# Kernel tuning notes

Hardware: AMD Instinct MI355X
Metric: run time of the kernel (lower is better)

The kernel has to match this reference:

```python
import jax, jax.numpy as jnp
import numpy as np
from jax import lax

B, LE, LD = 16, 512, 256
D, H, DFF = 512, 8, 2048
ENC_IN, DEC_IN, MARK, CO = 7, 7, 4, 7
NE, ND = 3, 2
TOPK = int((D // H) * 0.25)  # 16, from ProbSparseMultiheadAttention


def layer_norm(x, p):
    m = jnp.mean(x, -1, keepdims=True)
    v = jnp.mean((x - m) ** 2, -1, keepdims=True)
    return (x - m) / jnp.sqrt(v + 1e-5) * p[0] + p[1]


def attn(q, k, v, W, b, mask=None, topk=None):
    # W: [4, D, D] (q,k,v,o), b: [4, D]
    Bq, Lq, _ = q.shape
    dk = D // H
    Q = (q @ W[0] + b[0]).reshape(Bq, Lq, H, dk)
    K = (k @ W[1] + b[1]).reshape(Bq, -1, H, dk)
    V = (v @ W[2] + b[2]).reshape(Bq, -1, H, dk)
    s = jnp.einsum('bqhd,bkhd->bhqk', Q, K) / jnp.sqrt(jnp.float32(dk))
    if mask is not None:
        s = s + mask * (-1e9)
    if topk is not None:
        # ProbSparse: keep only top-k key scores per query before softmax
        kth = lax.top_k(s, topk)[0][..., -1:]
        s = jnp.where(s >= kth, s, -1e9)
    w = jax.nn.softmax(s, axis=-1)
    o = jnp.einsum('bhqk,bkhd->bqhd', w, V).reshape(Bq, Lq, D)
    return o @ W[3] + b[3]


def conv_distill(x, w, cb, g, bb):
    # x: [B, L, D]; circular-pad conv1d(k=3, pad=2) + BN(batch stats) + ELU + maxpool(k3,s2,p1)
    xc = jnp.transpose(x, (0, 2, 1))
    xp = jnp.pad(xc, ((0, 0), (0, 0), (2, 2)), mode='wrap')
    y = lax.conv_general_dilated(xp, w, (1,), 'VALID', dimension_numbers=('NCH', 'OIH', 'NCH')) + cb[None, :, None]
    m = jnp.mean(y, (0, 2), keepdims=True)
    v = jnp.var(y, (0, 2), keepdims=True)
    y = (y - m) / jnp.sqrt(v + 1e-5) * g[None, :, None] + bb[None, :, None]
    y = jax.nn.elu(y)
    y = lax.reduce_window(y, -jnp.inf, lax.max, (1, 1, 3), (1, 1, 2), ((0, 0), (0, 0), (1, 1)))
    return jnp.transpose(y, (0, 2, 1))


def setup_inputs() -> dict:
    key = jax.random.key(0)
    ks = iter(jax.random.split(key, 64))
    def nrm(shape, s=0.02):
        return jax.random.normal(next(ks), shape, dtype=jnp.float32) * s
    def ln_p(*lead):
        return jnp.stack([jnp.ones(lead + (D,), jnp.float32), jnp.zeros(lead + (D,), jnp.float32)], axis=len(lead))
    return {
        'x_enc': nrm((B, LE, ENC_IN), 1.0),
        'x_mark_enc': nrm((B, LE, MARK), 1.0),
        'x_dec': nrm((B, LD, DEC_IN), 1.0),
        'x_mark_dec': nrm((B, LD, MARK), 1.0),
        'enc_vw': nrm((ENC_IN, D)), 'enc_vb': jnp.zeros((D,)),
        'enc_mw': nrm((MARK, D)), 'enc_mb': jnp.zeros((D,)),
        'dec_vw': nrm((DEC_IN, D)), 'dec_vb': jnp.zeros((D,)),
        'dec_mw': nrm((MARK, D)), 'dec_mb': jnp.zeros((D,)),
        'eW': nrm((NE, 4, D, D)), 'eb': jnp.zeros((NE, 4, D)),
        'effw1': nrm((NE, D, DFF)), 'effb1': jnp.zeros((NE, DFF)),
        'effw2': nrm((NE, DFF, D)), 'effb2': jnp.zeros((NE, D)),
        'eln1': ln_p(NE), 'eln2': ln_p(NE),
        'cw': nrm((NE - 1, D, D, 3)), 'cb': jnp.zeros((NE - 1, D)),
        'cbn_g': jnp.ones((NE - 1, D)), 'cbn_b': jnp.zeros((NE - 1, D)),
        'enc_norm': ln_p(),
        'dsW': nrm((ND, 4, D, D)), 'dsb': jnp.zeros((ND, 4, D)),
        'dcW': nrm((ND, 4, D, D)), 'dcb': jnp.zeros((ND, 4, D)),
        'dffw1': nrm((ND, D, DFF)), 'dffb1': jnp.zeros((ND, DFF)),
        'dffw2': nrm((ND, DFF, D)), 'dffb2': jnp.zeros((ND, D)),
        'dln': ln_p(ND, 3),
        'dec_norm': ln_p(),
        'fcw': nrm((D, CO)), 'fcb': jnp.zeros((CO,)),
    }


def reference(x_enc, x_mark_enc, x_dec, x_mark_dec, enc_vw, enc_vb, enc_mw, enc_mb,
              dec_vw, dec_vb, dec_mw, dec_mb, eW, eb, effw1, effb1, effw2, effb2,
              eln1, eln2, cw, cb, cbn_g, cbn_b, enc_norm, dsW, dsb, dcW, dcb,
              dffw1, dffb1, dffw2, dffb2, dln, dec_norm, fcw, fcb):
    # embedding: value projection + temporal-mark projection
    x = x_enc @ enc_vw + enc_vb + x_mark_enc @ enc_mw + enc_mb
    # encoder: ProbSparse attn layers with conv distillation after the first NE-1
    for i in range(NE):
        a = attn(x, x, x, eW[i], eb[i], topk=TOPK)
        x = layer_norm(x + a, eln1[i])
        f = jax.nn.relu(x @ effw1[i] + effb1[i]) @ effw2[i] + effb2[i]
        x = layer_norm(x + f, eln2[i])
        if i < NE - 1:
            x = conv_distill(x, cw[i], cb[i], cbn_g[i], cbn_b[i])
    mem = layer_norm(x, enc_norm)
    # decoder
    y = x_dec @ dec_vw + dec_vb + x_mark_dec @ dec_mw + dec_mb
    cmask = jnp.triu(jnp.ones((LD, LD), jnp.float32), 1)[None, None]
    for i in range(ND):
        a = attn(y, y, y, dsW[i], dsb[i], mask=cmask)
        y = layer_norm(y + a, dln[i, 0])
        a = attn(y, mem, mem, dcW[i], dcb[i])
        y = layer_norm(y + a, dln[i, 1])
        f = jax.nn.relu(y @ dffw1[i] + dffb1[i]) @ dffw2[i] + dffb2[i]
        y = layer_norm(y + f, dln[i, 2])
    y = layer_norm(y, dec_norm)
    return y @ fcw + fcb
```

## Files before the change

### kernel.cpp

```cpp
#include <hip/hip_runtime.h>
#include <hip/hip_bf16.h>


#define DM 512
#define DK 64

using bf16 = __hip_bfloat16;
typedef short s8v __attribute__((ext_vector_type(8)));
typedef float f4v __attribute__((ext_vector_type(4)));

__device__ inline float b2f(bf16 x) { return __bfloat162float(x); }
__device__ inline float u2f(unsigned short u) { return __uint_as_float((unsigned)u << 16); }

__device__ inline float ldw(const void* p, unsigned i, int f) {
    return f ? b2f(((const bf16*)p)[i]) : ((const float*)p)[i];
}

__device__ inline unsigned f2ord(float s) {
    unsigned u = __float_as_uint(s);
    return u ^ ((unsigned)((int)u >> 31) | 0x80000000u);
}

__device__ inline int popc_lt(unsigned long long m) {
    return (int)__builtin_amdgcn_mbcnt_hi((unsigned)(m >> 32),
            __builtin_amdgcn_mbcnt_lo((unsigned)m, 0u));
}

__device__ inline void gl_lds16(const short* g, short* l) {
    __builtin_amdgcn_global_load_lds(
        (const __attribute__((address_space(1))) unsigned int*)g,
        (__attribute__((address_space(3))) unsigned int*)l,
        16, 0, 0);
}

__global__ __launch_bounds__(256) void sniff_k(const unsigned* __restrict__ x, int nwords,
                                               int* __restrict__ flag) {
    __shared__ int red[4];
    const int t = threadIdx.x;
    int c = 0;
    for (int i = t; i < nwords; i += 256) c += ((x[i] & 0x7F80u) == 0x3F80u) ? 1 : 0;
    #pragma unroll
    for (int o = 32; o > 0; o >>= 1) c += __shfl_down(c, o);
    __syncthreads();
    if ((t & 63) == 0) red[t >> 6] = c;
    __syncthreads();
    if (t == 0) flag[0] = (red[0] + red[1] + red[2] + red[3] > nwords / 20) ? 1 : 0;
}

__device__ inline float block_sum256(float v, float* red) {
    #pragma unroll
    for (int o = 32; o > 0; o >>= 1) v += __shfl_down(v, o);
    __syncthreads();
    if ((threadIdx.x & 63) == 0) red[threadIdx.x >> 6] = v;
    __syncthreads();
    return red[0] + red[1] + red[2] + red[3];
}

__global__ __launch_bounds__(256) void embed_k(
    const void* __restrict__ xv, const void* __restrict__ vw, const void* __restrict__ vb,
    const void* __restrict__ xm, const void* __restrict__ mw, const void* __restrict__ mb,
    bf16* __restrict__ Out, int rows, int Cv, int Cm, const int* __restrict__ flagp)
{
    const int f = *flagp;
    int i = blockIdx.x * 256 + threadIdx.x;
    if (i >= rows * DM) return;
    const int r = i >> 9, d = i & 511;
    float acc = ldw(vb, d, f) + ldw(mb, d, f);
    for (int c = 0; c < Cv; ++c) acc += ldw(xv, r * Cv + c, f) * ldw(vw, c * DM + d, f);
    for (int c = 0; c < Cm; ++c) acc += ldw(xm, r * Cm + c, f) * ldw(mw, c * DM + d, f);
    Out[i] = __float2bfloat16(acc);
}

__global__ __launch_bounds__(256) void transp_k(
    const void* __restrict__ W, unsigned off, unsigned zstride, bf16* __restrict__ out,
    int K, int N, const int* __restrict__ flagp)
{
    __shared__ float tile[32][33];
    const int f = *flagp;
    const unsigned zo = blockIdx.z * zstride;
    const int t = threadIdx.x;
    const int tx = t & 31, ty = t >> 5;
    const int n0 = blockIdx.x * 32, k0 = blockIdx.y * 32;
    #pragma unroll
    for (int i = 0; i < 4; ++i)
        tile[ty + 8 * i][tx] = ldw(W, off + zo + (unsigned)(k0 + ty + 8 * i) * N + n0 + tx, f);
    __syncthreads();
    #pragma unroll
    for (int i = 0; i < 4; ++i)
        out[(size_t)zo + (size_t)(n0 + ty + 8 * i) * K + k0 + tx] = __float2bfloat16(tile[tx][ty + 8 * i]);
}

template<bool G3, bool RELU>
__global__ __launch_bounds__(256) void mgemm_k(
    const short* __restrict__ A, const int* __restrict__ ridx,
    const short* __restrict__ Wt,
    const void* __restrict__ bias, unsigned boff0,
    bf16* __restrict__ C, int M, int N, int K, int lda, int ldc,
    const int* __restrict__ flagp)
{
    __shared__ short As[128 * 32];
    __shared__ short Ws[128 * 32];
    const int t = threadIdx.x;
    const int bm = blockIdx.y * 128, bn = blockIdx.x * 128;
    const int lane = t & 63, wave = t >> 6;
    const int mbase = (wave >> 1) * 64, nbase = (wave & 1) * 64;
    const int l15 = lane & 15, quad = lane >> 4;
    const int lrow = lane >> 2, lk = (lane & 3) * 8;

    f4v acc[4][4] = {};

    for (int k0 = 0; k0 < K; k0 += 32) {
        __syncthreads();
        #pragma unroll
        for (int j = 0; j < 2; ++j) {
            const int rb = wave * 32 + j * 16;
            const int row = bm + rb + lrow;
            const int rowc = row < M ? row : M - 1;
            const short* g;
            if (G3) {
                const int r = ridx[(k0 >> 9) * M + rowc];
                g = A + (size_t)r * lda + (k0 & 511) + lk;
            } else {
                g = A + (size_t)rowc * lda + k0 + lk;
            }
            gl_lds16(g, &As[rb * 32]);
        }
        #pragma unroll
        for (int j = 0; j < 2; ++j) {
            const int nb = wave * 32 + j * 16;
            gl_lds16(Wt + (size_t)(bn + nb + lrow) * K + k0 + lk, &Ws[nb * 32]);
        }
        __syncthreads();
        s8v af[4], bfv[4];
        #pragma unroll
        for (int i = 0; i < 4; ++i) {
            af[i]  = *(const s8v*)&As[(mbase + i * 16 + l15) * 32 + quad * 8];
            bfv[i] = *(const s8v*)&Ws[(nbase + i * 16 + l15) * 32 + quad * 8];
        }
        #pragma unroll
        for (int mi = 0; mi < 4; ++mi)
            #pragma unroll
            for (int ni = 0; ni < 4; ++ni)
                acc[mi][ni] = __builtin_amdgcn_mfma_f32_16x16x32_bf16(
                    af[mi], bfv[ni], acc[mi][ni], 0, 0, 0);
    }

    const int f = *flagp;
    float bv[4];
    #pragma unroll
    for (int ni = 0; ni < 4; ++ni)
        bv[ni] = ldw(bias, boff0 + (unsigned)(bn + nbase + ni * 16 + l15), f);

    #pragma unroll
    for (int mi = 0; mi < 4; ++mi) {
        #pragma unroll
        for (int r = 0; r < 4; ++r) {
            const int row = bm + mbase + mi * 16 + quad * 4 + r;
            if (row < M) {
                #pragma unroll
                for (int ni = 0; ni < 4; ++ni) {
                    float o = acc[mi][ni][r] + bv[ni];
                    if (RELU) o = fmaxf(o, 0.f);
                    C[(size_t)row * ldc + bn + nbase + ni * 16 + l15] = __float2bfloat16(o);
                }
            }
        }
    }
}

template<bool G3, bool RELU>
__global__ __launch_bounds__(256) void mgemm64_k(
    const short* __restrict__ A, const int* __restrict__ ridx,
    const short* __restrict__ Wt,
    const void* __restrict__ bias, unsigned boff0,
    bf16* __restrict__ C, int M, int N, int K, int lda, int ldc,
    const int* __restrict__ flagp)
{
    __shared__ short As[64 * 32];
    __shared__ short Ws[64 * 32];
    const int t = threadIdx.x;
    const int bm = blockIdx.y * 64, bn = blockIdx.x * 64;
    const int lane = t & 63, wave = t >> 6;
    const int mbase = (wave >> 1) * 32, nbase = (wave & 1) * 32;
    const int l15 = lane & 15, quad = lane >> 4;
    const int lrow = lane >> 2, lk = (lane & 3) * 8;

    f4v acc[2][2] = {};

    for (int k0 = 0; k0 < K; k0 += 32) {
        __syncthreads();
        {
            const int rb = wave * 16;
            const int row = bm + rb + lrow;
            const int rowc = row < M ? row : M - 1;
            const short* g;
            if (G3) {
                const int r = ridx[(k0 >> 9) * M + rowc];
                g = A + (size_t)r * lda + (k0 & 511) + lk;
            } else {
                g = A + (size_t)rowc * lda + k0 + lk;
            }
            gl_lds16(g, &As[rb * 32]);
        }
        {
            const int nb = wave * 16;
            gl_lds16(Wt + (size_t)(bn + nb + lrow) * K + k0 + lk, &Ws[nb * 32]);
        }
        __syncthreads();
        s8v af[2], bfv[2];
        #pragma unroll
        for (int i = 0; i < 2; ++i) {
            af[i]  = *(const s8v*)&As[(mbase + i * 16 + l15) * 32 + quad * 8];
            bfv[i] = *(const s8v*)&Ws[(nbase + i * 16 + l15) * 32 + quad * 8];
        }
        #pragma unroll
        for (int mi = 0; mi < 2; ++mi)
            #pragma unroll
            for (int ni = 0; ni < 2; ++ni)
                acc[mi][ni] = __builtin_amdgcn_mfma_f32_16x16x32_bf16(
                    af[mi], bfv[ni], acc[mi][ni], 0, 0, 0);
    }

    const int f = *flagp;
    float bv[2];
    #pragma unroll
    for (int ni = 0; ni < 2; ++ni)
        bv[ni] = ldw(bias, boff0 + (unsigned)(bn + nbase + ni * 16 + l15), f);

    #pragma unroll
    for (int mi = 0; mi < 2; ++mi) {
        #pragma unroll
        for (int r = 0; r < 4; ++r) {
            const int row = bm + mbase + mi * 16 + quad * 4 + r;
            if (row < M) {
                #pragma unroll
                for (int ni = 0; ni < 2; ++ni) {
                    float o = acc[mi][ni][r] + bv[ni];
                    if (RELU) o = fmaxf(o, 0.f);
                    C[(size_t)row * ldc + bn + nbase + ni * 16 + l15] = __float2bfloat16(o);
                }
            }
        }
    }
}

template<int MODE>
__global__ __launch_bounds__(512, 8) void fattn_k(
    bf16* __restrict__ q, const bf16* __restrict__ k, const bf16* __restrict__ v,
    int ldq, int ldkv, int Lq, int Lk)
{
    __shared__ short Qs[16 * 72];
    __shared__ float S[16 * 516];
    __shared__ int   PC[16][16];
    __shared__ float PE[16][16];

    const int t = threadIdx.x;
    const int q0 = blockIdx.x * 16, h = blockIdx.y, b = blockIdx.z;
    const int lane = t & 63, wave = t >> 6;
    const int l15 = lane & 15, quad = lane >> 4;

    const int qv = (Lq - q0) < 16 ? (Lq - q0) : 16;

    const bf16* Kbase = k + (size_t)b * Lk * ldkv + h * DK;
    const bf16* Vbase = v + (size_t)b * Lk * ldkv + h * DK;
    bf16* Qbase = q + (size_t)(b * Lq + q0) * ldq + h * DK;

    const int kmax = (MODE == 1) ? (q0 + 16 < Lk ? q0 + 16 : Lk) : Lk;
    const int ntile = (kmax + 63) >> 6;
    const int kpad = ntile << 6;
    const int nchunk = kpad >> 4;

    {
        const int qr = t >> 5;
        const int qsrc = qr < qv ? qr : qv - 1;
        *(ushort2*)&Qs[qr * 72 + (t & 31) * 2] =
            *(const ushort2*)(Qbase + (size_t)qsrc * ldq + (t & 31) * 2);
    }
    __syncthreads();

    {
        const s8v a0 = *(const s8v*)&Qs[l15 * 72 + quad * 8];
        const s8v a1 = *(const s8v*)&Qs[l15 * 72 + 32 + quad * 8];
        int c = wave;
        s8v b0, b1;
        if (c < nchunk) {
            int srow = c * 16 + l15; if (srow >= Lk) srow = Lk - 1;
            const bf16* kp = Kbase + (size_t)srow * ldkv + quad * 8;
            b0 = *(const s8v*)kp;
            b1 = *(const s8v*)(kp + 32);
        }
        while (c < nchunk) {
            const int cn = c + 8;
            s8v n0, n1;
            if (cn < nchunk) {
                int srow = cn * 16 + l15; if (srow >= Lk) srow = Lk - 1;
                const bf16* kp = Kbase + (size_t)srow * ldkv + quad * 8;
                n0 = *(const s8v*)kp;
                n1 = *(const s8v*)(kp + 32);
            }
            f4v acc = {0.f, 0.f, 0.f, 0.f};
            acc = __builtin_amdgcn_mfma_f32_16x16x32_bf16(a0, b0, acc, 0, 0, 0);
            acc = __builtin_amdgcn_mfma_f32_16x16x32_bf16(a1, b1, acc, 0, 0, 0);
            const int colg = c * 16 + l15;
            #pragma unroll
            for (int r = 0; r < 4; ++r) {
                const int qrow = quad * 4 + r;
                float s = acc[r] * 0.125f;
                if (colg >= Lk) s = -1e9f;
                if (MODE == 1 && colg > q0 + qrow) s = -1e9f;
                S[qrow * 516 + colg] = s;
            }
            b0 = n0; b1 = n1; c = cn;
        }
    }
    __syncthreads();

    const int rowA = wave, rowB = wave + 8;
    float aA = 0.f, aB = 0.f;
    float invA, invB;
    if (MODE == 0) {
        unsigned keyA[8], keyB[8];
        #pragma unroll
        for (int j = 0; j < 8; ++j) {
            const int col = lane + 64 * j;
            const bool ok = col < kpad;
            keyA[j] = ok ? ((f2ord(S[rowA * 516 + col]) & 0xFFFFFE00u) | (unsigned)col) : 0u;
            keyB[j] = ok ? ((f2ord(S[rowB * 516 + col]) & 0xFFFFFE00u) | (unsigned)col) : 0u;
        }
        unsigned kmA = keyA[0], kmB = keyB[0];
        #pragma unroll
        for (int j = 1; j < 8; ++j) {
            kmA = kmA > keyA[j] ? kmA : keyA[j];
            kmB = kmB > keyB[j] ? kmB : keyB[j];
        }
        #pragma unroll
        for (int off = 1; off < 64; off <<= 1) {
            const unsigned oA = __shfl_xor(kmA, off);
            const unsigned oB = __shfl_xor(kmB, off);
            kmA = kmA > oA ? kmA : oA;
            kmB = kmB > oB ? kmB : oB;
        }
        const float mrA = S[rowA * 516 + (int)(kmA & 511u)];
        const float mrB = S[rowB * 516 + (int)(kmB & 511u)];

        unsigned TA = 0u, TB = 0u;
        bool dA = false, dB = false;
        for (int bbit = 31; bbit >= 0; --bbit) {
            if (!dA) {
                const unsigned T2 = TA | (1u << bbit);
                int c = 0;
                #pragma unroll
                for (int j = 0; j < 8; ++j)
                    c += (int)__popcll(__ballot(keyA[j] >= T2));
                if (c >= 16) { TA = T2; dA = (c == 16); }
            }
            if (!dB) {
                const unsigned T2 = TB | (1u << bbit);
                int c = 0;
                #pragma unroll
                for (int j = 0; j < 8; ++j)
                    c += (int)__popcll(__ballot(keyB[j] >= T2));
                if (c >= 16) { TB = T2; dB = (c == 16); }
            }
            if (dA && dB) break;
        }

        int cntA = 0, cntB = 0;
        #pragma unroll
        for (int j = 0; j < 8; ++j) {
            const bool sA = keyA[j] >= TA;
            const unsigned long long balA = __ballot(sA);
            if (sA) {
                const int p = cntA + popc_lt(balA);
                const int col = (int)(keyA[j] & 511u);
                PC[rowA][p] = col;
                PE[rowA][p] = expf(S[rowA * 516 + col] - mrA);
            }
            cntA += (int)__popcll(balA);
            const bool sB = keyB[j] >= TB;
            const unsigned long long balB = __ballot(sB);
            if (sB) {
                const int p = cntB + popc_lt(balB);
                const int col = (int)(keyB[j] & 511u);
                PC[rowB][p] = col;
                PE[rowB][p] = expf(S[rowB * 516 + col] - mrB);
            }
            cntB += (int)__popcll(balB);
        }

        float denA = 0.f, denB = 0.f;
        #pragma unroll
        for (int it = 0; it < 16; ++it) {
            const int cA = PC[rowA][it];
            const float eA = PE[rowA][it];
            denA += eA;
            aA += eA * b2f(Vbase[(size_t)cA * ldkv + lane]);
            const int cB = PC[rowB][it];
            const float eB = PE[rowB][it];
            denB += eB;
            aB += eB * b2f(Vbase[(size_t)cB * ldkv + lane]);
        }
        invA = 1.f / denA;
        invB = 1.f / denB;
    } else {
        float lvA = -INFINITY, lvB = -INFINITY;
        #pragma unroll
        for (int j = 0; j < 8; ++j) {
            const int col = lane + 64 * j;
            if (col < kpad) {
                lvA = fmaxf(lvA, S[rowA * 516 + col]);
                lvB = fmaxf(lvB, S[rowB * 516 + col]);
            }
        }
        #pragma unroll
        for (int off = 1; off < 64; off <<= 1) {
            lvA = fmaxf(lvA, __shfl_xor(lvA, off));
            lvB = fmaxf(lvB, __shfl_xor(lvB, off));
        }
        float pA = 0.f, pB = 0.f;
        #pragma unroll
        for (int j = 0; j < 8; ++j) {
            const int col = lane + 64 * j;
            if (col < kpad) {
                const float wA = expf(S[rowA * 516 + col] - lvA);
                const float wB = expf(S[rowB * 516 + col] - lvB);
                S[rowA * 516 + col] = wA;
                S[rowB * 516 + col] = wB;
                pA += wA; pB += wB;
            }
        }
        #pragma unroll
        for (int off = 1; off < 64; off <<= 1) {
            pA += __shfl_xor(pA, off);
            pB += __shfl_xor(pB, off);
        }
        invA = 1.f / pA;
        invB = 1.f / pB;
        #pragma unroll 8
        for (int k2 = 0; k2 < kmax; ++k2) {
            const float vv = b2f(Vbase[(size_t)k2 * ldkv + lane]);
            aA += S[rowA * 516 + k2] * vv;
            aB += S[rowB * 516 + k2] * vv;
        }
    }
    if (rowA < qv)
        Qbase[(size_t)rowA * ldq + lane] = __float2bfloat16(aA * invA);
    if (rowB < qv)
        Qbase[(size_t)rowB * ldq + lane] = __float2bfloat16(aB * invB);
}

__global__ __launch_bounds__(256) void ln_off_k(
    const bf16* __restrict__ X, const bf16* __restrict__ R,
    const void* __restrict__ gb, unsigned goff,
    bf16* __restrict__ Out, const int* __restrict__ flagp)
{
    __shared__ float red[4];
    const int f = *flagp;
    const int t = threadIdx.x;
    const size_t base = (size_t)blockIdx.x * DM;
    float v0 = b2f(X[base + t]), v1 = b2f(X[base + t + 256]);
    if (R) { v0 += b2f(R[base + t]); v1 += b2f(R[base + t + 256]); }
    const float mean = block_sum256(v0 + v1, red) * (1.f / 512.f);
    const float d0 = v0 - mean, d1 = v1 - mean;
    const float var = block_sum256(d0 * d0 + d1 * d1, red) * (1.f / 512.f);
    const float rstd = rsqrtf(var + 1e-5f);
    Out[base + t]       = __float2bfloat16(d0 * rstd * ldw(gb, goff + t, f)       + ldw(gb, goff + 512 + t, f));
    Out[base + t + 256] = __float2bfloat16(d1 * rstd * ldw(gb, goff + t + 256, f) + ldw(gb, goff + 768 + t, f));
}

__global__ __launch_bounds__(256) void convw_k(const void* __restrict__ w,
                                               bf16* __restrict__ wt, int total,
                                               const int* __restrict__ flagp) {
    const int f = *flagp;
    int i = blockIdx.x * 256 + threadIdx.x;
    if (i >= total) return;
    const int layer = i / 786432, rem2 = i % 786432;
    const int o = rem2 / 1536, rem = rem2 % 1536;
    const int j = rem >> 9, c = rem & 511;
    wt[i] = __float2bfloat16(ldw(w, (unsigned)layer * 786432u + (unsigned)(o * 512 + c) * 3 + j, f));
}

__global__ __launch_bounds__(256) void convidx_k(int* __restrict__ idx, int Lc, int L, int total) {
    int i = blockIdx.x * 256 + threadIdx.x;
    if (i >= total) return;
    const int j = i / (16 * Lc), mrem = i % (16 * Lc);
    const int b = mrem / Lc, l = mrem % Lc;
    int src = l + j - 2;
    src %= L; if (src < 0) src += L;
    idx[i] = b * L + src;
}

__global__ __launch_bounds__(256) void bnstat1_k(const bf16* __restrict__ Y, float* __restrict__ part, int M) {
    const int t = threadIdx.x;
    float s0 = 0.f, q0 = 0.f, s1 = 0.f, q1 = 0.f;
    for (int r = blockIdx.x; r < M; r += gridDim.x) {
        const ushort2 u = *reinterpret_cast<const ushort2*>(Y + (size_t)r * DM + t * 2);
        const float a = u2f(u.x), c = u2f(u.y);
        s0 += a; q0 += a * a;
        s1 += c; q1 += c * c;
    }
    float* p = part + (size_t)blockIdx.x * 1024;
    p[2 * t] = s0; p[2 * t + 1] = s1;
    p[512 + 2 * t] = q0; p[512 + 2 * t + 1] = q1;
}

__global__ __launch_bounds__(256) void bnstat2_k(const float* __restrict__ part, float* __restrict__ stats,
                                                 int nchunk, int M) {
    const int ch = blockIdx.x * 256 + threadIdx.x;
    if (ch >= 512) return;
    float S = 0.f, Qs = 0.f;
    for (int c = 0; c < nchunk; ++c) { S += part[c * 1024 + ch]; Qs += part[c * 1024 + 512 + ch]; }
    const float mean = S / (float)M;
    const float var = Qs / (float)M - mean * mean;
    stats[ch] = mean;
    stats[512 + ch] = fmaxf(var, 0.f);
}

__global__ __launch_bounds__(256) void bnpool_k(
    const bf16* __restrict__ Yc, const float* __restrict__ stats,
    const void* __restrict__ g, const void* __restrict__ bb, unsigned off,
    bf16* __restrict__ Out, int Lc, int Lout, int total, const int* __restrict__ flagp)
{
    const int f = *flagp;
    int i = blockIdx.x * 256 + threadIdx.x;
    if (i >= total) return;
    const int ch = i & 511;
    const int lp = (i >> 9) % Lout;
    const int b = i / (512 * Lout);
    const float mean = stats[ch], var = stats[512 + ch];
    const float sc = ldw(g, off + ch, f) * rsqrtf(var + 1e-5f);
    const float sh = ldw(bb, off + ch, f) - mean * sc;
    float mx = -INFINITY;
    const int l0 = 2 * lp - 1;
    #pragma unroll
    for (int d = 0; d < 3; ++d) {
        const int l = l0 + d;
        if (l >= 0 && l < Lc) {
            float v = b2f(Yc[((size_t)b * Lc + l) * DM + ch]) * sc + sh;
            v = v > 0.f ? v : expm1f(v);
            mx = fmaxf(mx, v);
        }
    }
    Out[((size_t)b * Lout + lp) * DM + ch] = __float2bfloat16(mx);
}

__global__ __launch_bounds__(256) void fc_k(
    const bf16* __restrict__ Yn, const void* __restrict__ fcw, const void* __restrict__ fcb,
    void* __restrict__ out, int total, const int* __restrict__ flagp)
{
    const int f = *flagp;
    int i = blockIdx.x * 256 + threadIdx.x;
    if (i >= total) return;
    const int r = i / 7, co = i % 7;
    const bf16* yr = Yn + (size_t)r * DM;
    float acc = ldw(fcb, co, f);
    for (int d = 0; d < DM; ++d) acc += b2f(yr[d]) * ldw(fcw, d * 7 + co, f);
    if (f) ((bf16*)out)[i] = __float2bfloat16(acc);
    else   ((float*)out)[i] = acc;
}

extern "C" void kernel_launch(void* const* d_in, const int* in_sizes, int n_in,
                              void* d_out, int out_size, void* d_ws, size_t ws_size,
                              hipStream_t stream)
{
    const void* x_enc      = d_in[0];
    const void* x_mark_enc = d_in[1];
    const void* x_dec      = d_in[2];
    const void* x_mark_dec = d_in[3];
    const void* enc_vw = d_in[4];
    const void* enc_vb = d_in[5];
    const void* enc_mw = d_in[6];
    const void* enc_mb = d_in[7];
    const void* dec_vw = d_in[8];
    const void* dec_vb = d_in[9];
    const void* dec_mw = d_in[10];
    const void* dec_mb = d_in[11];
    const void* eW    = d_in[12];
    const void* ebi   = d_in[13];
    const void* effw1 = d_in[14];
    const void* effb1 = d_in[15];
    const void* effw2 = d_in[16];
    const void* effb2 = d_in[17];
    const void* eln1  = d_in[18];
    const void* eln2  = d_in[19];
    const void* cw    = d_in[20];
    const void* cb    = d_in[21];
    const void* cbn_g = d_in[22];
    const void* cbn_b = d_in[23];
    const void* enc_norm = d_in[24];
    const void* dsW   = d_in[25];
    const void* dsb   = d_in[26];
    const void* dcW   = d_in[27];
    const void* dcb   = d_in[28];
    const void* dffw1 = d_in[29];
    const void* dffb1 = d_in[30];
    const void* dffw2 = d_in[31];
    const void* dffb2 = d_in[32];
    const void* dln   = d_in[33];
    const void* dec_norm = d_in[34];
    const void* fcw   = d_in[35];
    const void* fcb   = d_in[36];

    char* wsp = (char*)d_ws;
    bf16* X    = (bf16*)wsp;
    bf16* QKV  = (bf16*)(wsp + ((size_t)8 << 20));
    bf16* HID  = QKV;
    bf16* OUT  = (bf16*)(wsp + ((size_t)40 << 20));
    bf16* WT   = (bf16*)(wsp + ((size_t)48 << 20));
    int*   IDX0 = (int*)(wsp + ((size_t)88 << 20));
    int*   IDX1 = IDX0 + 24672;
    float* PART = (float*)(wsp + ((size_t)89 << 20));
    float* STATS= (float*)(wsp + ((size_t)89 << 20) + (1 << 18));
    int*   FLAG = (int*)(wsp + ((size_t)89 << 20) + (1 << 18) + 4096);
    bf16* MEMb = X;
    bf16* Yd   = (bf16*)(wsp + (size_t)16 * 130 * 512 * 2);

    bf16* WTE  = WT;
    bf16* EW1T = WT + 3145728;
    bf16* EW2T = WT + 6291456;
    bf16* CWT  = WT + 9437184;
    bf16* DSWt = WT + 11010048;
    bf16* DCWt = WT + 13107200;
    bf16* DW1T = WT + 15204352;
    bf16* DW2T = WT + 17301504;

    auto cdiv = [](int a, int b) { return (a + b - 1) / b; };
    auto gemm = [&](const bf16* A, const bf16* Wt, const void* bias, unsigned boff,
                    bf16* C, int M, int N, int K, int lda, int ldc, bool relu) {
        dim3 g(N / 128, cdiv(M, 128));
        if (relu) mgemm_k<false, true><<<g, 256, 0, stream>>>(
            (const short*)A, nullptr, (const short*)Wt, bias, boff, C, M, N, K, lda, ldc, FLAG);
        else      mgemm_k<false, false><<<g, 256, 0, stream>>>(
            (const short*)A, nullptr, (const short*)Wt, bias, boff, C, M, N, K, lda, ldc, FLAG);
    };
    auto gemm64 = [&](const bf16* A, const bf16* Wt, const void* bias, unsigned boff,
                      bf16* C, int M, int N, int K, int lda, int ldc, bool relu) {
        dim3 g(N / 64, cdiv(M, 64));
        if (relu) mgemm64_k<false, true><<<g, 256, 0, stream>>>(
            (const short*)A, nullptr, (const short*)Wt, bias, boff, C, M, N, K, lda, ldc, FLAG);
        else      mgemm64_k<false, false><<<g, 256, 0, stream>>>(
            (const short*)A, nullptr, (const short*)Wt, bias, boff, C, M, N, K, lda, ldc, FLAG);
    };
    auto transp = [&](const void* W, unsigned zstride, int nz, bf16* out, int K, int N) {
        transp_k<<<dim3(N / 32, K / 32, nz), 256, 0, stream>>>(W, 0u, zstride, out, K, N, FLAG);
    };

    sniff_k<<<1, 256, 0, stream>>>((const unsigned*)x_mark_enc, 16384, FLAG);
    transp(eW,    262144u, 12, WTE,  512, 512);
    transp(effw1, 1048576u, 3, EW1T, 512, 2048);
    transp(effw2, 1048576u, 3, EW2T, 2048, 512);
    convw_k<<<cdiv(1572864, 256), 256, 0, stream>>>(cw, CWT, 1572864, FLAG);
    transp(dsW,   262144u, 8, DSWt, 512, 512);
    transp(dcW,   262144u, 8, DCWt, 512, 512);
    transp(dffw1, 1048576u, 2, DW1T, 512, 2048);
    transp(dffw2, 1048576u, 2, DW2T, 2048, 512);
    convidx_k<<<cdiv(24672, 256), 256, 0, stream>>>(IDX0, 514, 512, 24672);
    convidx_k<<<cdiv(12432, 256), 256, 0, stream>>>(IDX1, 259, 257, 12432);
    embed_k<<<cdiv(16 * 512 * 512, 256), 256, 0, stream>>>(
        x_enc, enc_vw, enc_vb, x_mark_enc, enc_mw, enc_mb, X, 16 * 512, 7, 4, FLAG);

    int L = 512;
    for (int i = 0; i < 3; ++i) {
        const int rows = 16 * L;
        const unsigned b0 = (unsigned)i * 4u * 512u;
        if (i == 0) gemm(X, WTE + (size_t)i * 4 * 262144, ebi, b0, QKV, rows, 1536, 512, 512, 1536, false);
        else      gemm64(X, WTE + (size_t)i * 4 * 262144, ebi, b0, QKV, rows, 1536, 512, 512, 1536, false);
        fattn_k<0><<<dim3(cdiv(L, 16), 8, 16), 512, 0, stream>>>(
            QKV, QKV + 512, QKV + 1024, 1536, 1536, L, L);
        gemm64(QKV, WTE + (size_t)(i * 4 + 3) * 262144, ebi, b0 + 1536u, OUT, rows, 512, 512, 1536, 512, false);
        ln_off_k<<<rows, 256, 0, stream>>>(X, OUT, eln1, (unsigned)i * 1024u, X, FLAG);

        if (i == 0) gemm(X, EW1T + (size_t)i * 1048576, effb1, (unsigned)i * 2048u, HID, rows, 2048, 512, 512, 2048, true);
        else      gemm64(X, EW1T + (size_t)i * 1048576, effb1, (unsigned)i * 2048u, HID, rows, 2048, 512, 512, 2048, true);
        gemm64(HID, EW2T + (size_t)i * 1048576, effb2, (unsigned)i * 512u, OUT, rows, 512, 2048, 2048, 512, false);
        ln_off_k<<<rows, 256, 0, stream>>>(X, OUT, eln2, (unsigned)i * 1024u, X, FLAG);

        if (i < 2) {
            const int Lc = L + 2, Mc = 16 * Lc;
            const int* IDXi = (i == 0) ? IDX0 : IDX1;
            mgemm64_k<true, false><<<dim3(8, cdiv(Mc, 64)), 256, 0, stream>>>(
                (const short*)X, IDXi, (const short*)(CWT + (size_t)i * 786432),
                cb, (unsigned)i * 512u, QKV, Mc, 512, 1536, 512, 512, FLAG);
            bnstat1_k<<<32, 256, 0, stream>>>(QKV, PART, Mc);
            bnstat2_k<<<2, 256, 0, stream>>>(PART, STATS, 32, Mc);
            const int Lout = (L + 1) / 2 + 1;
            const int tot = 16 * Lout * 512;
            bnpool_k<<<cdiv(tot, 256), 256, 0, stream>>>(
                QKV, STATS, cbn_g, cbn_b, (unsigned)i * 512u, X, Lc, Lout, tot, FLAG);
            L = Lout;
        }
    }
    const int Lm = L;
    ln_off_k<<<16 * Lm, 256, 0, stream>>>(X, nullptr, enc_norm, 0u, MEMb, FLAG);

    const int rowsD = 16 * 256;
    embed_k<<<cdiv(rowsD * 512, 256), 256, 0, stream>>>(
        x_dec, dec_vw, dec_vb, x_mark_dec, dec_mw, dec_mb, Yd, rowsD, 7, 4, FLAG);

    bf16* CQ  = QKV;
    bf16* CKV = QKV + (size_t)4096 * 512;
    for (int i = 0; i < 2; ++i) {
        const unsigned b0 = (unsigned)i * 4u * 512u;
        gemm64(Yd, DSWt + (size_t)i * 4 * 262144, dsb, b0, QKV, rowsD, 1536, 512, 512, 1536, false);
        fattn_k<1><<<dim3(16, 8, 16), 512, 0, stream>>>(
            QKV, QKV + 512, QKV + 1024, 1536, 1536, 256, 256);
        gemm64(QKV, DSWt + (size_t)(i * 4 + 3) * 262144, dsb, b0 + 1536u, OUT, rowsD, 512, 512, 1536, 512, false);
        ln_off_k<<<rowsD, 256, 0, stream>>>(Yd, OUT, dln, (unsigned)(i * 3 + 0) * 1024u, Yd, FLAG);

        gemm64(Yd, DCWt + (size_t)i * 4 * 262144, dcb, b0, CQ, rowsD, 512, 512, 512, 512, false);
        gemm64(MEMb, DCWt + (size_t)(i * 4 + 1) * 262144, dcb, b0 + 512u, CKV, 16 * Lm, 1024, 512, 512, 1024, false);
        fattn_k<2><<<dim3(16, 8, 16), 512, 0, stream>>>(
            CQ, CKV, CKV + 512, 512, 1024, 256, Lm);
        gemm64(CQ, DCWt + (size_t)(i * 4 + 3) * 262144, dcb, b0 + 1536u, OUT, rowsD, 512, 512, 512, 512, false);
        ln_off_k<<<rowsD, 256, 0, stream>>>(Yd, OUT, dln, (unsigned)(i * 3 + 1) * 1024u, Yd, FLAG);

        gemm64(Yd, DW1T + (size_t)i * 1048576, dffb1, (unsigned)i * 2048u, HID, rowsD, 2048, 512, 512, 2048, true);
        gemm64(HID, DW2T + (size_t)i * 1048576, dffb2, (unsigned)i * 512u, OUT, rowsD, 512, 2048, 2048, 512, false);
        ln_off_k<<<rowsD, 256, 0, stream>>>(Yd, OUT, dln, (unsigned)(i * 3 + 2) * 1024u, Yd, FLAG);
    }

    ln_off_k<<<rowsD, 256, 0, stream>>>(Yd, nullptr, dec_norm, 0u, OUT, FLAG);
    fc_k<<<cdiv(rowsD * 7, 256), 256, 0, stream>>>(OUT, fcw, fcb, d_out, rowsD * 7, FLAG);
}
```

Before: 1.443 ms.

## Double-buffer LDS tiles in MFMA GEMM kernels to overlap loads with compute

Both the 128x128 and 64x64 MFMA GEMM kernels now keep two LDS buffers for A and W tiles. The next K-slice is issued via global-to-LDS loads before computing on the current one, with one barrier per iteration instead of two. The aim is to hide global load latency behind MFMA work and cut synchronisation. It doubles shared memory per block, which may reduce occupancy. Correctness depends on the async LDS loads being complete when the barrier is reached.

```diff
diff --git a/kernel.cpp b/kernel.cpp
--- a/kernel.cpp
+++ b/kernel.cpp
@@ -98,8 +98,8 @@
     bf16* __restrict__ C, int M, int N, int K, int lda, int ldc,
     const int* __restrict__ flagp)
 {
-    __shared__ short As[128 * 32];
-    __shared__ short Ws[128 * 32];
+    __shared__ short As[2][128 * 32];
+    __shared__ short Ws[2][128 * 32];
     const int t = threadIdx.x;
     const int bm = blockIdx.y * 128, bn = blockIdx.x * 128;
     const int lane = t & 63, wave = t >> 6;
@@ -109,8 +109,7 @@
 
     f4v acc[4][4] = {};
 
-    for (int k0 = 0; k0 < K; k0 += 32) {
-        __syncthreads();
+    auto stage = [&](int buf, int k0) {
         #pragma unroll
         for (int j = 0; j < 2; ++j) {
             const int rb = wave * 32 + j * 16;
@@ -123,19 +122,26 @@
             } else {
                 g = A + (size_t)rowc * lda + k0 + lk;
             }
-            gl_lds16(g, &As[rb * 32]);
+            gl_lds16(g, &As[buf][rb * 32]);
         }
         #pragma unroll
         for (int j = 0; j < 2; ++j) {
             const int nb = wave * 32 + j * 16;
-            gl_lds16(Wt + (size_t)(bn + nb + lrow) * K + k0 + lk, &Ws[nb * 32]);
-        }
-        __syncthreads();
+            gl_lds16(Wt + (size_t)(bn + nb + lrow) * K + k0 + lk, &Ws[buf][nb * 32]);
+        }
+    };
+
+    const int nt = K >> 5;
+    stage(0, 0);
+    __syncthreads();
+    for (int it = 0; it < nt; ++it) {
+        if (it + 1 < nt) stage((it + 1) & 1, (it + 1) << 5);
+        const int cb = it & 1;
         s8v af[4], bfv[4];
         #pragma unroll
         for (int i = 0; i < 4; ++i) {
-            af[i]  = *(const s8v*)&As[(mbase + i * 16 + l15) * 32 + quad * 8];
-            bfv[i] = *(const s8v*)&Ws[(nbase + i * 16 + l15) * 32 + quad * 8];
+            af[i]  = *(const s8v*)&As[cb][(mbase + i * 16 + l15) * 32 + quad * 8];
+            bfv[i] = *(const s8v*)&Ws[cb][(nbase + i * 16 + l15) * 32 + quad * 8];
         }
         #pragma unroll
         for (int mi = 0; mi < 4; ++mi)
@@ -143,6 +149,7 @@
             for (int ni = 0; ni < 4; ++ni)
                 acc[mi][ni] = __builtin_amdgcn_mfma_f32_16x16x32_bf16(
                     af[mi], bfv[ni], acc[mi][ni], 0, 0, 0);
+        if (it + 1 < nt) __syncthreads();
     }
 
     const int f = *flagp;
@@ -176,8 +183,8 @@
     bf16* __restrict__ C, int M, int N, int K, int lda, int ldc,
     const int* __restrict__ flagp)
 {
-    __shared__ short As[64 * 32];
-    __shared__ short Ws[64 * 32];
+    __shared__ short As[2][64 * 32];
+    __shared__ short Ws[2][64 * 32];
     const int t = threadIdx.x;
     const int bm = blockIdx.y * 64, bn = blockIdx.x * 64;
     const int lane = t & 63, wave = t >> 6;
@@ -187,8 +194,7 @@
 
     f4v acc[2][2] = {};
 
-    for (int k0 = 0; k0 < K; k0 += 32) {
-        __syncthreads();
+    auto stage = [&](int buf, int k0) {
         {
             const int rb = wave * 16;
             const int row = bm + rb + lrow;
@@ -200,18 +206,25 @@
             } else {
                 g = A + (size_t)rowc * lda + k0 + lk;
             }
-            gl_lds16(g, &As[rb * 32]);
+            gl_lds16(g, &As[buf][rb * 32]);
         }
         {
             const int nb = wave * 16;
-            gl_lds16(Wt + (size_t)(bn + nb + lrow) * K + k0 + lk, &Ws[nb * 32]);
-        }
-        __syncthreads();
+            gl_lds16(Wt + (size_t)(bn + nb + lrow) * K + k0 + lk, &Ws[buf][nb * 32]);
+        }
+    };
+
+    const int nt = K >> 5;
+    stage(0, 0);
+    __syncthreads();
+    for (int it = 0; it < nt; ++it) {
+        if (it + 1 < nt) stage((it + 1) & 1, (it + 1) << 5);
+        const int cb = it & 1;
         s8v af[2], bfv[2];
         #pragma unroll
         for (int i = 0; i < 2; ++i) {
-            af[i]  = *(const s8v*)&As[(mbase + i * 16 + l15) * 32 + quad * 8];
-            bfv[i] = *(const s8v*)&Ws[(nbase + i * 16 + l15) * 32 + quad * 8];
+            af[i]  = *(const s8v*)&As[cb][(mbase + i * 16 + l15) * 32 + quad * 8];
+            bfv[i] = *(const s8v*)&Ws[cb][(nbase + i * 16 + l15) * 32 + quad * 8];
         }
         #pragma unroll
         for (int mi = 0; mi < 2; ++mi)
@@ -219,6 +232,7 @@
             for (int ni = 0; ni < 2; ++ni)
                 acc[mi][ni] = __builtin_amdgcn_mfma_f32_16x16x32_bf16(
                     af[mi], bfv[ni], acc[mi][ni], 0, 0, 0);
+        if (it + 1 < nt) __syncthreads();
     }
 
     const int f = *flagp;
```

Result: no change. 1.451 ms (+0.5%).
